# Kernel optimization log

Measured on AMD Instinct MI355X. Metric: run time of the kernel, lower is better.

The kernel has to match this reference:

```python
import jax, jax.numpy as jnp
import numpy as np

D = 1024

def setup_inputs() -> dict:
    key = jax.random.key(0)
    ks = jax.random.split(key, 9)
    s = 1.0 / np.sqrt(D)
    x = jax.random.normal(ks[0], (4096, 8, D), dtype=jnp.float32)
    Wq = jax.random.uniform(ks[1], (D, D), jnp.float32, -s, s)
    bq = jax.random.uniform(ks[2], (D,), jnp.float32, -s, s)
    Wk = jax.random.uniform(ks[3], (D, D), jnp.float32, -s, s)
    bk = jax.random.uniform(ks[4], (D,), jnp.float32, -s, s)
    Wv = jax.random.uniform(ks[5], (D, D), jnp.float32, -s, s)
    bv = jax.random.uniform(ks[6], (D,), jnp.float32, -s, s)
    Wo = jax.random.uniform(ks[7], (D, D), jnp.float32, -s, s)
    bo = jax.random.uniform(ks[8], (D,), jnp.float32, -s, s)
    return {"x": x, "Wq": Wq, "bq": bq, "Wk": Wk, "bk": bk,
            "Wv": Wv, "bv": bv, "Wo": Wo, "bo": bo}

def reference(x, Wq, bq, Wk, bk, Wv, bv, Wo, bo):
    # x: (S, B, D) seq-first, matching torch module
    Q = jax.nn.elu(x @ Wq.T + bq) + 1.0  # (S,B,D)
    K = jax.nn.elu(x @ Wk.T + bk) + 1.0  # (S,B,D)
    V = x @ Wv.T + bv                    # (S,B,D)
    # KV = K^T V per batch: (B, D, D)
    KV = jnp.einsum('sbd,sbe->bde', K, V)
    # out = Q @ KV per batch, back to (S,B,D)
    out = jnp.einsum('sbd,bde->sbe', Q, KV)
    return out @ Wo.T + bo
```

## Files before the change

### kernel.cpp

```cpp
#include <hip/hip_runtime.h>


typedef __bf16 bf16;
typedef __attribute__((ext_vector_type(8))) __bf16 bf16x8;
typedef __attribute__((ext_vector_type(4))) __bf16 bf16x4;
typedef __attribute__((ext_vector_type(4))) float f32x4;

static constexpr int S = 4096;
static constexpr int B = 8;
static constexpr int D = 1024;
static constexpr int SB = S * B;
static constexpr long long NELEM = (long long)SB * D;

__device__ __forceinline__ void load_lds16(const bf16* g, void* l)
{
    __builtin_amdgcn_global_load_lds(
        (const __attribute__((address_space(1))) void*)g,
        (__attribute__((address_space(3))) void*)l, 16, 0, 0);
}

__global__ void cvt_f32_to_bf16(const float* __restrict__ in, bf16* __restrict__ out, int n)
{
    int i = (blockIdx.x * blockDim.x + threadIdx.x) * 4;
    int stride = gridDim.x * blockDim.x * 4;
    for (; i < n; i += stride) {
        float4 v = *(const float4*)(in + i);
        bf16x4 o;
        o[0] = (bf16)v.x; o[1] = (bf16)v.y; o[2] = (bf16)v.z; o[3] = (bf16)v.w;
        *(bf16x4*)(out + i) = o;
    }
}

template<int BM, int BN, int WM, int WN, int EPI, int OUTF32, int BIASROW>
__global__ __launch_bounds__(WM * WN * 64, 2) void gemm_bt(
    const bf16* __restrict__ A, const bf16* __restrict__ Bm,
    const float* __restrict__ bias, void* __restrict__ Cout,
    int lda, int ldb, int ldc, int K,
    long long aBatch, long long bBatch, long long cBatch)
{
    constexpr int THREADS = WM * WN * 64;
    constexpr int WROWS = BM / WM, WCOLS = BN / WN;
    constexpr int MI = WROWS / 16, NI = WCOLS / 16;
    constexpr int ABYTES = BM * 64;
    constexpr int BBYTES = BN * 64;
    constexpr int BUF = ABYTES + BBYTES;

    __shared__ unsigned char smem[4 * BUF];

    const int tid  = threadIdx.x;
    const int lane = tid & 63;
    const int wave = tid >> 6;
    const int wr   = wave / WN;
    const int wc   = wave % WN;
    const int bz   = blockIdx.z;

    const int nx  = gridDim.x;
    const int bid = blockIdx.y * nx + blockIdx.x;
    const int cpx = (nx * gridDim.y) >> 3;
    const int swz = (bid & 7) * cpx + (bid >> 3);
    const long long m0 = (long long)(swz / nx) * BM;
    const long long n0 = (long long)(swz % nx) * BN;

    const bf16* Ab = A  + bz * aBatch + m0 * lda;
    const bf16* Bb = Bm + bz * bBatch + n0 * ldb;

    f32x4 acc[MI][NI] = {};

    const int NT = K >> 5;

    auto stage = [&](int t) {
        unsigned char* dst = smem + (t & 3) * BUF;
        const long long kk = (long long)t << 5;
        #pragma unroll
        for (int j = 0; j < 2; ++j) {
            const int g  = wave * 64 + lane + j * THREADS;
            const int gs = g ^ ((g >> 3) & 3);
            const int row = gs >> 2, col = (gs & 3) * 8;
            load_lds16(Ab + (long long)row * lda + kk + col,
                       dst + (wave * 64 + j * THREADS) * 16);
        }
        #pragma unroll
        for (int j = 0; j < 2; ++j) {
            const int g  = wave * 64 + lane + j * THREADS;
            const int gs = g ^ ((g >> 3) & 3);
            const int row = gs >> 2, col = (gs & 3) * 8;
            load_lds16(Bb + (long long)row * ldb + kk + col,
                       dst + ABYTES + (wave * 64 + j * THREADS) * 16);
        }
    };

    stage(0); stage(1); stage(2);

    const int ko2 = (lane >> 4) * 16;
    const int la15 = lane & 15;

    for (int t = 0; t < NT; ++t) {
        if (t + 2 < NT)      asm volatile("s_waitcnt vmcnt(8)" ::: "memory");
        else if (t + 1 < NT) asm volatile("s_waitcnt vmcnt(4)" ::: "memory");
        else                 asm volatile("s_waitcnt vmcnt(0)" ::: "memory");
        __builtin_amdgcn_s_barrier();
        asm volatile("" ::: "memory");

        if (t + 3 < NT) stage(t + 3);

        const unsigned char* buf = smem + (t & 3) * BUF;
        bf16x8 a[MI], b[NI];
        #pragma unroll
        for (int mi = 0; mi < MI; ++mi) {
            int ad = (wr * WROWS + mi * 16 + la15) * 64 + ko2;
            ad ^= ((ad >> 7) & 3) << 4;
            a[mi] = *(const bf16x8*)(buf + ad);
        }
        #pragma unroll
        for (int ni = 0; ni < NI; ++ni) {
            int ad = (wc * WCOLS + ni * 16 + la15) * 64 + ko2;
            ad ^= ((ad >> 7) & 3) << 4;
            b[ni] = *(const bf16x8*)(buf + ABYTES + ad);
        }

        __builtin_amdgcn_s_setprio(1);
        #pragma unroll
        for (int mi = 0; mi < MI; ++mi)
            #pragma unroll
            for (int ni = 0; ni < NI; ++ni)
                acc[mi][ni] = __builtin_amdgcn_mfma_f32_16x16x32_bf16(
                    a[mi], b[ni], acc[mi][ni], 0, 0, 0);
        __builtin_amdgcn_s_setprio(0);
    }

    const int crow = (lane >> 4) * 4;
    const int ccol = lane & 15;
    #pragma unroll
    for (int ni = 0; ni < NI; ++ni) {
        const long long c = n0 + wc * WCOLS + ni * 16 + ccol;
        float bcol = 0.0f;
        if (!BIASROW && bias) bcol = bias[c];
        #pragma unroll
        for (int mi = 0; mi < MI; ++mi) {
            const long long r0 = m0 + wr * WROWS + mi * 16 + crow;
            #pragma unroll
            for (int j = 0; j < 4; ++j) {
                float v = acc[mi][ni][j];
                v += BIASROW ? bias[r0 + j] : bcol;
                if (EPI == 1) v = (v > 0.0f) ? (v + 1.0f) : __expf(v);
                const long long idx = bz * cBatch + (r0 + j) * ldc + c;
                if (OUTF32) ((float*)Cout)[idx] = v;
                else        ((bf16*)Cout)[idx]  = (bf16)v;
            }
        }
    }
}

extern "C" void kernel_launch(void* const* d_in, const int* in_sizes, int n_in,
                              void* d_out, int out_size, void* d_ws, size_t ws_size,
                              hipStream_t stream)
{
    const float* x  = (const float*)d_in[0];
    const float* Wq = (const float*)d_in[1];
    const float* bq = (const float*)d_in[2];
    const float* Wk = (const float*)d_in[3];
    const float* bk = (const float*)d_in[4];
    const float* Wv = (const float*)d_in[5];
    const float* bv = (const float*)d_in[6];
    const float* Wo = (const float*)d_in[7];
    const float* bo = (const float*)d_in[8];
    float* out = (float*)d_out;

    char* ws = (char*)d_ws;
    if (ws_size < (size_t)159383552) return;
    bf16* xb   = (bf16*)(ws + 0);
    bf16* KVWT = (bf16*)(ws + 0);
    bf16* Qb   = (bf16*)(ws + 67108864);
    bf16* KV   = (bf16*)(ws + 134217728);
    bf16* wqb  = (bf16*)(ws + 150994944);
    bf16* wkb  = wqb + 1048576;
    bf16* wvb  = wkb + 1048576;
    bf16* wob  = wvb + 1048576;
    bf16* Kt   = (bf16*)d_out;
    bf16* Vt   = Kt + NELEM;

    cvt_f32_to_bf16<<<4096, 256, 0, stream>>>(x,  xb,  (int)NELEM);
    cvt_f32_to_bf16<<<1024, 256, 0, stream>>>(Wq, wqb, D * D);
    cvt_f32_to_bf16<<<1024, 256, 0, stream>>>(Wk, wkb, D * D);
    cvt_f32_to_bf16<<<1024, 256, 0, stream>>>(Wv, wvb, D * D);
    cvt_f32_to_bf16<<<1024, 256, 0, stream>>>(Wo, wob, D * D);

    gemm_bt<256, 256, 2, 4, 1, 0, 0><<<dim3(4, 128, 1), 512, 0, stream>>>(
        xb, wqb, bq, Qb, D, D, D, D, 0, 0, 0);

    gemm_bt<256, 256, 2, 4, 1, 0, 1><<<dim3(16, 4, 8), 512, 0, stream>>>(
        wkb, xb, bk, Kt, D, B * D, S, D, 0, (long long)D, (long long)D * S);

    gemm_bt<256, 256, 2, 4, 0, 0, 1><<<dim3(16, 4, 8), 512, 0, stream>>>(
        wvb, xb, bv, Vt, D, B * D, S, D, 0, (long long)D, (long long)D * S);

    gemm_bt<128, 128, 2, 2, 0, 0, 0><<<dim3(8, 8, 8), 256, 0, stream>>>(
        Kt, Vt, nullptr, KV, S, S, D, S,
        (long long)D * S, (long long)D * S, (long long)D * D);

    gemm_bt<128, 128, 2, 2, 0, 0, 0><<<dim3(8, 8, 8), 256, 0, stream>>>(
        wob, KV, nullptr, KVWT, D, D, D, D,
        0, (long long)D * D, (long long)D * D);

    gemm_bt<256, 256, 2, 4, 0, 1, 0><<<dim3(4, 16, 8), 512, 0, stream>>>(
        Qb, KVWT, bo, out, B * D, D, B * D, D,
        (long long)D, (long long)D * D, (long long)D);
}
```

Measured before the change: 523.7 us.

## Fold Wo into V projection and add 8-phase pipelined 256x256 GEMM kernel

Precomputes Wvo = Wo·Wv and bias bvo = Wo·bv, so V is projected directly into the output space. This removes the batched KV×Wo GEMM (8 batches of 1024³). It also adds a new 256x256 GEMM with a 128KB LDS, double-buffered K-halves and fine-grained interleaving of loads and MFMAs, and uses it for the large projection and output GEMMs. The cost is one small extra D×D GEMM plus a transpose and bias kernel, a reordered KV product, and extra bf16 rounding from the prefused weight.

```diff
diff --git a/kernel.cpp b/kernel.cpp
--- a/kernel.cpp
+++ b/kernel.cpp
@@ -31,6 +31,50 @@
     }
 }
 
+__global__ __launch_bounds__(256) void cvt_transpose_1024(
+    const float* __restrict__ in, bf16* __restrict__ out)
+{
+    __shared__ bf16 tile[64][72];
+    const int e0 = blockIdx.y * 64;
+    const int d0 = blockIdx.x * 64;
+    const int t  = threadIdx.x;
+    const int rl = t >> 3;
+    const int c8 = (t & 7) * 8;
+    #pragma unroll
+    for (int p = 0; p < 2; ++p) {
+        int r = rl + p * 32;
+        float4 v0 = *(const float4*)(in + (long long)(e0 + r) * D + d0 + c8);
+        float4 v1 = *(const float4*)(in + (long long)(e0 + r) * D + d0 + c8 + 4);
+        tile[c8+0][r] = (bf16)v0.x; tile[c8+1][r] = (bf16)v0.y;
+        tile[c8+2][r] = (bf16)v0.z; tile[c8+3][r] = (bf16)v0.w;
+        tile[c8+4][r] = (bf16)v1.x; tile[c8+5][r] = (bf16)v1.y;
+        tile[c8+6][r] = (bf16)v1.z; tile[c8+7][r] = (bf16)v1.w;
+    }
+    __syncthreads();
+    #pragma unroll
+    for (int p = 0; p < 2; ++p) {
+        int dr = rl + p * 32;
+        *(bf16x8*)(out + (long long)(d0 + dr) * D + e0 + c8) = *(bf16x8*)(&tile[dr][c8]);
+    }
+}
+
+__global__ __launch_bounds__(256) void bvo_kernel(
+    const float* __restrict__ Wo, const float* __restrict__ bv, float* __restrict__ bvo)
+{
+    const int row = blockIdx.x;
+    const int t = threadIdx.x;
+    float4 w = *(const float4*)(Wo + (long long)row * D + t * 4);
+    float4 b = *(const float4*)(bv + t * 4);
+    float s = w.x*b.x + w.y*b.y + w.z*b.z + w.w*b.w;
+    __shared__ float red[256];
+    red[t] = s; __syncthreads();
+    for (int off = 128; off > 0; off >>= 1) {
+        if (t < off) red[t] += red[t + off];
+        __syncthreads();
+    }
+    if (t == 0) bvo[row] = red[0];
+}
+
 template<int BM, int BN, int WM, int WN, int EPI, int OUTF32, int BIASROW>
 __global__ __launch_bounds__(WM * WN * 64, 2) void gemm_bt(
     const bf16* __restrict__ A, const bf16* __restrict__ Bm,
@@ -65,7 +109,6 @@
     const bf16* Bb = Bm + bz * bBatch + n0 * ldb;
 
     f32x4 acc[MI][NI] = {};
-
     const int NT = K >> 5;
 
     auto stage = [&](int t) {
@@ -138,6 +181,147 @@
         #pragma unroll
         for (int mi = 0; mi < MI; ++mi) {
             const long long r0 = m0 + wr * WROWS + mi * 16 + crow;
+            #pragma unroll
+            for (int j = 0; j < 4; ++j) {
+                float v = acc[mi][ni][j];
+                v += BIASROW ? bias[r0 + j] : bcol;
+                if (EPI == 1) v = (v > 0.0f) ? (v + 1.0f) : __expf(v);
+                const long long idx = bz * cBatch + (r0 + j) * ldc + c;
+                if (OUTF32) ((float*)Cout)[idx] = v;
+                else        ((bf16*)Cout)[idx]  = (bf16)v;
+            }
+        }
+    }
+}
+
+template<int EPI, int OUTF32, int BIASROW>
+__global__ __launch_bounds__(512, 1) void gemm8p(
+    const bf16* __restrict__ A, const bf16* __restrict__ Bm,
+    const float* __restrict__ bias, void* __restrict__ Cout,
+    int lda, int ldb, int ldc, int K,
+    long long aBatch, long long bBatch, long long cBatch)
+{
+    __shared__ unsigned char smem[131072];
+
+    const int tid  = threadIdx.x;
+    const int lane = tid & 63;
+    const int wave = tid >> 6;
+    const int wr   = wave >> 2;
+    const int wc   = wave & 3;
+    const int bz   = blockIdx.z;
+
+    const int nx  = gridDim.x;
+    const int bid = blockIdx.y * nx + blockIdx.x;
+    const int cpx = (nx * gridDim.y) >> 3;
+    const int swzb = (bid & 7) * cpx + (bid >> 3);
+    const long long m0 = (long long)(swzb / nx) * 256;
+    const long long n0 = (long long)(swzb % nx) * 256;
+
+    const bf16* Ab = A  + bz * aBatch + m0 * lda;
+    const bf16* Bb = Bm + bz * bBatch + n0 * ldb;
+
+    const int sg = (lane & 3) ^ ((lane >> 3) & 3);
+    const long long srow = wave * 32 + (lane >> 2);
+    const bf16* srcA = Ab + srow * lda + sg * 8;
+    const bf16* srcB = Bb + srow * ldb + sg * 8;
+    const int dstoff = wave * 2048;
+
+    const int la15 = lane & 15;
+    const int rsw  = (lane >> 4) ^ ((la15 >> 1) & 3);
+    const int a16  = (wr * 128 + la15) * 4 + rsw;
+    const int b16  = (wc * 64  + la15) * 4 + rsw;
+
+    f32x4 acc[8][4] = {};
+    const int NT = K >> 6;
+    const int NI = NT >> 1;
+
+    auto stageA = [&](int T, int kh) {
+        const int reg = ((((T & 1) << 1) | kh) << 14);
+        const long long kp = ((long long)T << 6) + (kh << 5);
+        load_lds16(srcA + kp,            smem + reg + dstoff);
+        load_lds16(srcA + kp + 16 * lda, smem + reg + dstoff + 1024);
+    };
+    auto stageB = [&](int T, int kh) {
+        const int reg = 65536 + ((((T & 1) << 1) | kh) << 14);
+        const long long kp = ((long long)T << 6) + (kh << 5);
+        load_lds16(srcB + kp,            smem + reg + dstoff);
+        load_lds16(srcB + kp + 16 * ldb, smem + reg + dstoff + 1024);
+    };
+
+    stageB(0, 0); stageA(0, 0); stageB(0, 1); stageA(0, 1);
+    stageB(1, 0); stageA(1, 0); stageB(1, 1);
+    asm volatile("s_waitcnt vmcnt(10)" ::: "memory");
+    __builtin_amdgcn_s_barrier();
+    __builtin_amdgcn_sched_barrier(0);
+
+    bf16x8 bfr[4];
+    for (int i = 0; i < NI; ++i) {
+        const int t = 2 * i;
+        const bool nl = (i + 1 < NI);
+        #pragma unroll
+        for (int p = 0; p < 8; ++p) {
+            const int ks  = (p >> 1) & 1;
+            const int ch  = p & 1;
+            const int buf = p >> 2;
+            const int regA = ((buf << 1) | ks) << 14;
+            const int regB = 65536 + regA;
+
+            bf16x8 afr[4];
+            if (ch == 0) {
+                #pragma unroll
+                for (int ni = 0; ni < 4; ++ni)
+                    bfr[ni] = *(const bf16x8*)(smem + regB + (b16 + ni * 64) * 16);
+            }
+            #pragma unroll
+            for (int m4 = 0; m4 < 4; ++m4)
+                afr[m4] = *(const bf16x8*)(smem + regA + (a16 + (ch * 4 + m4) * 64) * 16);
+
+            if      (p == 0) stageA(t + 1, 1);
+            else if (p == 1) { if (t + 2 < NT) stageB(t + 2, 0); }
+            else if (p == 2) { if (t + 2 < NT) stageA(t + 2, 0); }
+            else if (p == 3) { if (t + 2 < NT) stageB(t + 2, 1); }
+            else if (p == 4) { if (t + 2 < NT) stageA(t + 2, 1); }
+            else if (p == 5) { if (t + 3 < NT) stageB(t + 3, 0); }
+            else if (p == 6) { if (t + 3 < NT) stageA(t + 3, 0); }
+            else             { if (t + 3 < NT) stageB(t + 3, 1); }
+
+            if (p == 1) {
+                if (nl) asm volatile("s_waitcnt vmcnt(10)" ::: "memory");
+                else    asm volatile("s_waitcnt vmcnt(8)"  ::: "memory");
+            } else if (p == 3) {
+                if (nl) asm volatile("s_waitcnt vmcnt(10)" ::: "memory");
+                else    asm volatile("s_waitcnt vmcnt(4)"  ::: "memory");
+            } else if (p == 5) {
+                if (nl) asm volatile("s_waitcnt vmcnt(10)" ::: "memory");
+                else    asm volatile("s_waitcnt vmcnt(0)"  ::: "memory");
+            } else if (p == 7) {
+                if (nl) asm volatile("s_waitcnt vmcnt(10)" ::: "memory");
+            }
+
+            __builtin_amdgcn_s_barrier();
+            asm volatile("s_waitcnt lgkmcnt(0)" ::: "memory");
+            __builtin_amdgcn_s_setprio(1);
+            #pragma unroll
+            for (int m4 = 0; m4 < 4; ++m4)
+                #pragma unroll
+                for (int ni = 0; ni < 4; ++ni)
+                    acc[ch * 4 + m4][ni] = __builtin_amdgcn_mfma_f32_16x16x32_bf16(
+                        afr[m4], bfr[ni], acc[ch * 4 + m4][ni], 0, 0, 0);
+            __builtin_amdgcn_s_setprio(0);
+            __builtin_amdgcn_s_barrier();
+            __builtin_amdgcn_sched_barrier(0);
+        }
+    }
+
+    const int crow = (lane >> 4) * 4;
+    #pragma unroll
+    for (int ni = 0; ni < 4; ++ni) {
+        const long long c = n0 + wc * 64 + ni * 16 + la15;
+        float bcol = 0.0f;
+        if (!BIASROW && bias) bcol = bias[c];
+        #pragma unroll
+        for (int mi = 0; mi < 8; ++mi) {
+            const long long r0 = m0 + wr * 128 + mi * 16 + crow;
             #pragma unroll
             for (int j = 0; j < 4; ++j) {
                 float v = acc[mi][ni][j];
@@ -168,41 +352,42 @@
 
     char* ws = (char*)d_ws;
     if (ws_size < (size_t)159383552) return;
-    bf16* xb   = (bf16*)(ws + 0);
-    bf16* KVWT = (bf16*)(ws + 0);
-    bf16* Qb   = (bf16*)(ws + 67108864);
-    bf16* KV   = (bf16*)(ws + 134217728);
-    bf16* wqb  = (bf16*)(ws + 150994944);
-    bf16* wkb  = wqb + 1048576;
-    bf16* wvb  = wkb + 1048576;
-    bf16* wob  = wvb + 1048576;
-    bf16* Kt   = (bf16*)d_out;
-    bf16* Vt   = Kt + NELEM;
+    bf16*  xb   = (bf16*)(ws + 0);
+    bf16*  Qb   = (bf16*)(ws + 67108864);
+    bf16*  Wvo  = (bf16*)(ws + 67108864);
+    float* bvo  = (float*)(ws + 67108864 + 2097152);
+    bf16*  KVo  = (bf16*)(ws + 134217728);
+    bf16*  wqb  = (bf16*)(ws + 150994944);
+    bf16*  wkb  = wqb + 1048576;
+    bf16*  wob  = wkb + 1048576;
+    bf16*  wvT  = wob + 1048576;
+    bf16*  Kt   = (bf16*)d_out;
+    bf16*  Vt   = Kt + NELEM;
 
     cvt_f32_to_bf16<<<4096, 256, 0, stream>>>(x,  xb,  (int)NELEM);
     cvt_f32_to_bf16<<<1024, 256, 0, stream>>>(Wq, wqb, D * D);
     cvt_f32_to_bf16<<<1024, 256, 0, stream>>>(Wk, wkb, D * D);
-    cvt_f32_to_bf16<<<1024, 256, 0, stream>>>(Wv, wvb, D * D);
     cvt_f32_to_bf16<<<1024, 256, 0, stream>>>(Wo, wob, D * D);
-
-    gemm_bt<256, 256, 2, 4, 1, 0, 0><<<dim3(4, 128, 1), 512, 0, stream>>>(
+    cvt_transpose_1024<<<dim3(16, 16), 256, 0, stream>>>(Wv, wvT);
+    bvo_kernel<<<1024, 256, 0, stream>>>(Wo, bv, bvo);
+
+    gemm_bt<128, 128, 2, 2, 0, 0, 0><<<dim3(8, 8, 1), 256, 0, stream>>>(
+        wob, wvT, nullptr, Wvo, D, D, D, D, 0, 0, 0);
+
+    gemm8p<1, 0, 1><<<dim3(16, 4, 8), 512, 0, stream>>>(
+        wkb, xb, bk, Kt, D, B * D, S, D, 0, (long long)D, (long long)D * S);
+
+    gemm8p<0, 0, 1><<<dim3(16, 4, 8), 512, 0, stream>>>(
+        Wvo, xb, bvo, Vt, D, B * D, S, D, 0, (long long)D, (long long)D * S);
+
+    gemm8p<1, 0, 0><<<dim3(4, 128, 1), 512, 0, stream>>>(
         xb, wqb, bq, Qb, D, D, D, D, 0, 0, 0);
 
-    gemm_bt<256, 256, 2, 4, 1, 0, 1><<<dim3(16, 4, 8), 512, 0, stream>>>(
-        wkb, xb, bk, Kt, D, B * D, S, D, 0, (long long)D, (long long)D * S);
-
-    gemm_bt<256, 256, 2, 4, 0, 0, 1><<<dim3(16, 4, 8), 512, 0, stream>>>(
-        wvb, xb, bv, Vt, D, B * D, S, D, 0, (long long)D, (long long)D * S);
-
     gemm_bt<128, 128, 2, 2, 0, 0, 0><<<dim3(8, 8, 8), 256, 0, stream>>>(
-        Kt, Vt, nullptr, KV, S, S, D, S,
+        Vt, Kt, nullptr, KVo, S, S, D, S,
         (long long)D * S, (long long)D * S, (long long)D * D);
 
-    gemm_bt<128, 128, 2, 2, 0, 0, 0><<<dim3(8, 8, 8), 256, 0, stream>>>(
-        wob, KV, nullptr, KVWT, D, D, D, D,
-        0, (long long)D * D, (long long)D * D);
-
-    gemm_bt<256, 256, 2, 4, 0, 1, 0><<<dim3(4, 16, 8), 512, 0, stream>>>(
-        Qb, KVWT, bo, out, B * D, D, B * D, D,
+    gemm8p<0, 1, 0><<<dim3(4, 16, 8), 512, 0, stream>>>(
+        Qb, KVo, bo, out, B * D, D, B * D, D,
         (long long)D, (long long)D * D, (long long)D);
 }
```

Result: faster. 509.8 us (-2.6%).
